# Optimization experiments

Measured on AMD Instinct MI355X. Metric: run time of the kernel, lower is better.

The kernel has to match this reference:

```python
import jax, jax.numpy as jnp
import numpy as np

B, N, DN = 8, 4096, 64
E = 1048576
H, DM = 128, 64   # message MLP: 2*DN -> H -> DM
HU, F = 128, 64   # node-update MLP: DN+DM -> HU -> F


def setup_inputs() -> dict:
    key = jax.random.key(0)
    ks = jax.random.split(key, 13)
    inp = {
        'node_feats': jax.random.normal(ks[0], (B, N, DN), dtype=jnp.float32),
        'edge_b': jax.random.randint(ks[1], (E,), 0, B, dtype=jnp.int32),
        'edge_src': jax.random.randint(ks[2], (E,), 0, N, dtype=jnp.int32),
        'edge_dst': jax.random.randint(ks[3], (E,), 0, N, dtype=jnp.int32),
        'edge_vals': jax.random.uniform(ks[4], (E,), dtype=jnp.float32),
        # message MLP params (Dense-relu, Dense-linear)
        'Wm1': jax.random.normal(ks[5], (2 * DN, H), dtype=jnp.float32) / np.sqrt(2 * DN),
        'bm1': jnp.zeros((H,), jnp.float32),
        'Wm2': jax.random.normal(ks[6], (H, DM), dtype=jnp.float32) / np.sqrt(H),
        'bm2': jnp.zeros((DM,), jnp.float32),
        # node-update MLP params
        'Wu1': jax.random.normal(ks[7], (DN + DM, HU), dtype=jnp.float32) / np.sqrt(DN + DM),
        'bu1': jnp.zeros((HU,), jnp.float32),
        'Wu2': jax.random.normal(ks[8], (HU, F), dtype=jnp.float32) / np.sqrt(HU),
        'bu2': jnp.zeros((F,), jnp.float32),
    }
    return inp


def reference(node_feats, edge_b, edge_src, edge_dst, edge_vals,
              Wm1, bm1, Wm2, bm2, Wu1, bu1, Wu2, bu2):
    # --- create messages: gather src/target feats per edge ---
    src_feats = node_feats[edge_b, edge_src]            # (E, DN)
    tgt_feats = node_feats[edge_b, edge_dst]            # (E, DN)
    feats = jnp.concatenate([src_feats, tgt_feats], axis=-1)  # (E, 2*DN)
    h = jax.nn.relu(feats @ Wm1 + bm1)
    messages = h @ Wm2 + bm2                            # (E, DM)

    # --- gather (scatter) messages: weighted ragged segment-mean ---
    weighted = messages * edge_vals[:, None]            # (E, DM)
    seg = edge_b * N + edge_src                          # rowids b*max_N + src
    sums = jax.ops.segment_sum(weighted, seg, num_segments=B * N)
    counts = jax.ops.segment_sum(jnp.ones((E,), weighted.dtype), seg,
                                 num_segments=B * N)
    gathered = sums / jnp.maximum(counts, 1.0)[:, None]  # mean; 0 for empty rows
    gathered = gathered.reshape(B, N, DM)

    # --- update nodes ---
    upd_in = jnp.concatenate([node_feats, gathered], axis=-1)  # (B, N, DN+DM)
    hu = jax.nn.relu(upd_in @ Wu1 + bu1)
    updated = hu @ Wu2 + bu2                            # (B, N, F)
    return updated
```

## Files before the change

kernel.cpp:

```cpp
#include <hip/hip_runtime.h>

#define NB 8
#define NN 4096
#define DNF 64
#define NEDGE 1048576
#define DM 64
#define FF 64

#define NBKT2 2048
#define SPB2 16
#define NXCD 8
#define SUBCAP 176
#define OVFCAP 32768

using f32x4 = __attribute__((ext_vector_type(4))) float;
using s16x8 = __attribute__((ext_vector_type(8))) short;

__device__ __forceinline__ unsigned short f2b(float f) {
    union { float f; unsigned u; } v; v.f = f;
    unsigned r = (v.u + 0x7fffu + ((v.u >> 16) & 1u)) >> 16;
    return (unsigned short)r;
}
__device__ __forceinline__ float uif(unsigned u) {
    union { unsigned u; float f; } v; v.u = u;
    return v.f;
}

__device__ __forceinline__ void pack_one(const float* __restrict__ W,
                                         unsigned short* __restrict__ out,
                                         int K, int Ncols, int idx) {
    int j = idx & 7;
    int lane = (idx >> 3) & 63;
    int frag = idx >> 9;
    int KS = K >> 5;
    int ks = frag % KS;
    int nt = frag / KS;
    int k = ks * 32 + ((lane >> 4) << 3) + j;
    int col = nt * 16 + (lane & 15);
    out[idx] = f2b(W[k * Ncols + col]);
}

__global__ void pack_all(const float* __restrict__ Wm1, const float* __restrict__ Wm2,
                         const float* __restrict__ Wu1, const float* __restrict__ Wu2,
                         unsigned short* __restrict__ Qw, unsigned short* __restrict__ Pw,
                         unsigned short* __restrict__ Wm2p,
                         unsigned short* __restrict__ Wu1p, unsigned short* __restrict__ Wu2p) {
    int idx = blockIdx.x * 256 + threadIdx.x;
    if (idx < 8192)        pack_one(Wm1,              Qw,   64, 128, idx);
    else if (idx < 16384)  pack_one(Wm1 + 64 * 128,   Pw,   64, 128, idx - 8192);
    else if (idx < 24576)  pack_one(Wm2,              Wm2p, 128, 64, idx - 16384);
    else if (idx < 40960)  pack_one(Wu1,              Wu1p, 128, 128, idx - 24576);
    else                   pack_one(Wu2,              Wu2p, 128, 64, idx - 40960);
}

__global__ void pack_weights(const float* __restrict__ W, unsigned short* __restrict__ out,
                             int K, int Ncols) {
    int idx = blockIdx.x * 256 + threadIdx.x;
    if (idx >= K * Ncols) return;
    pack_one(W, out, K, Ncols, idx);
}

__launch_bounds__(256, 4)
__global__ void precompute_pq(const float* __restrict__ X,
                              const unsigned short* __restrict__ Qw,
                              const unsigned short* __restrict__ Pw,
                              const float* __restrict__ b1,
                              unsigned short* __restrict__ Qp,
                              unsigned short* __restrict__ Pp) {
    __shared__ unsigned short A[64][72];
    const int tid = threadIdx.x;
    const int g0 = blockIdx.x * 64;
    for (int i = 0; i < 16; ++i) {
        int idx = i * 256 + tid;
        int node = idx >> 6;
        int f = idx & 63;
        A[node][f] = f2b(X[(size_t)(g0 + node) * DNF + f]);
    }
    __syncthreads();
    const int wave = tid >> 6, lane = tid & 63;
    const int lr = lane & 15, lq = lane >> 4;
    const int arow = wave * 16 + lr;
    s16x8 a[2];
#pragma unroll
    for (int ks = 0; ks < 2; ++ks)
        a[ks] = *reinterpret_cast<const s16x8*>(&A[arow][ks * 32 + lq * 8]);
#pragma unroll
    for (int nt = 0; nt < 8; ++nt) {
        f32x4 accQ = {0.f, 0.f, 0.f, 0.f};
        f32x4 accP = {0.f, 0.f, 0.f, 0.f};
#pragma unroll
        for (int ks = 0; ks < 2; ++ks) {
            s16x8 bq = *reinterpret_cast<const s16x8*>(&Qw[(((nt << 1) + ks) * 64 + lane) * 8]);
            s16x8 bp = *reinterpret_cast<const s16x8*>(&Pw[(((nt << 1) + ks) * 64 + lane) * 8]);
            accQ = __builtin_amdgcn_mfma_f32_16x16x32_bf16(a[ks], bq, accQ, 0, 0, 0);
            accP = __builtin_amdgcn_mfma_f32_16x16x32_bf16(a[ks], bp, accP, 0, 0, 0);
        }
        int col = nt * 16 + lr;
        float bias = b1[col];
#pragma unroll
        for (int j = 0; j < 4; ++j) {
            int row = g0 + wave * 16 + lq * 4 + j;
            Qp[(size_t)row * 128 + col] = f2b(accQ[j] + bias);
            Pp[(size_t)row * 128 + col] = f2b(accP[j]);
        }
    }
}

__launch_bounds__(256, 8)
__global__ void scatter_xcd(const int* __restrict__ eb, const int* __restrict__ esrc,
                            const int* __restrict__ edst, const float* __restrict__ evals,
                            unsigned* __restrict__ gcurP, unsigned* __restrict__ payslot,
                            unsigned* __restrict__ ovf_cnt, unsigned* __restrict__ ovf_seg,
                            unsigned* __restrict__ ovf_pay) {
    unsigned xcd;
    asm volatile("s_getreg_b32 %0, hwreg(HW_REG_XCC_ID)" : "=s"(xcd));
    xcd &= (NXCD - 1);
    const int t0 = blockIdx.x * 1024 + threadIdx.x;
    int seg[4]; unsigned pk[4];
#pragma unroll
    for (int k = 0; k < 4; ++k) {
        int e = t0 + k * 256;
        seg[k] = eb[e] * NN + esrc[e];
        unsigned wq = (unsigned)fminf(evals[e] * 8192.0f + 0.5f, 8191.0f);
        pk[k] = (unsigned)edst[e] | (wq << 12) | ((unsigned)(seg[k] & 15) << 25);
    }
    unsigned pos[4];
#pragma unroll
    for (int k = 0; k < 4; ++k)
        pos[k] = atomicAdd(&gcurP[(xcd * NBKT2 + (seg[k] >> 4)) * 16], 1u);
#pragma unroll
    for (int k = 0; k < 4; ++k) {
        if (pos[k] < (unsigned)SUBCAP) {
            payslot[((size_t)(seg[k] >> 4) * NXCD + xcd) * SUBCAP + pos[k]] = pk[k];
        } else {
            unsigned o = atomicAdd(ovf_cnt, 1u);
            if (o < (unsigned)OVFCAP) { ovf_seg[o] = (unsigned)seg[k]; ovf_pay[o] = pk[k]; }
        }
    }
}

__launch_bounds__(256, 6)
__global__ void bucket16_fused(const unsigned short* __restrict__ Qp,
                               const unsigned short* __restrict__ Pp,
                               const unsigned* __restrict__ payslot,
                               const unsigned* __restrict__ gcurP,
                               const unsigned* __restrict__ ovf_cnt,
                               const unsigned* __restrict__ ovf_seg,
                               const unsigned* __restrict__ ovf_pay,
                               const unsigned short* __restrict__ Wm2p,
                               const float* __restrict__ b2m,
                               const float* __restrict__ X,
                               const unsigned short* __restrict__ Wu1p,
                               const float* __restrict__ bu1,
                               const unsigned short* __restrict__ Wu2p,
                               const float* __restrict__ bu2,
                               float* __restrict__ out) {
    __shared__ unsigned raw[NXCD * SUBCAP];
    __shared__ unsigned sorted[NXCD * SUBCAP];
    __shared__ unsigned short S[16][136];
    __shared__ unsigned short A1[16][136];
    __shared__ unsigned short Hs[16][136];
    __shared__ unsigned h4[4][16];
    __shared__ unsigned curb4[4][16];
    __shared__ unsigned offs[17];
    __shared__ unsigned cx[NXCD];
    __shared__ float SW[16], SC[16];
    const int tid = threadIdx.x, wv = tid >> 6, lane = tid & 63;
    const int bkt = (blockIdx.x & 7) * 256 + (blockIdx.x >> 3);
    const int node0 = bkt * SPB2;
    const int rowbase = (bkt >> 8) << 12;
    const unsigned novf = ovf_cnt[0];

#pragma unroll
    for (int i = 0; i < 4; ++i) {
        int idx = i * 256 + tid;
        int row = idx >> 6, f = idx & 63;
        A1[row][f] = f2b(X[(size_t)(node0 + row) * DNF + f]);
    }
    if (tid < 64) ((unsigned*)h4)[tid] = 0;
    if (tid < NXCD) cx[tid] = min(gcurP[(tid * NBKT2 + bkt) * 16], (unsigned)SUBCAP);
    __syncthreads();
#pragma unroll
    for (int xi = 0; xi < 2; ++xi) {
        int x = wv * 2 + xi;
        unsigned c = cx[x];
        for (unsigned i = lane; i < c; i += 64) {
            unsigned v = payslot[((size_t)bkt * NXCD + x) * SUBCAP + i];
            raw[x * SUBCAP + i] = v;
            atomicAdd(&h4[wv][(v >> 25) & 15u], 1u);
        }
    }
    __syncthreads();
    if (tid < 16) {
        int xx = (int)(h4[0][tid] + h4[1][tid] + h4[2][tid] + h4[3][tid]);
#pragma unroll
        for (int o = 1; o < 16; o <<= 1) {
            int y = __shfl_up(xx, o);
            if (tid >= o) xx += y;
        }
        offs[tid + 1] = (unsigned)xx;
        if (tid == 0) offs[0] = 0;
    }
    __syncthreads();
    if (tid < 64) {
        int w = tid >> 4, b = tid & 15;
        unsigned base = offs[b];
        for (int w2 = 0; w2 < w; ++w2) base += h4[w2][b];
        curb4[w][b] = base;
    }
    __syncthreads();
#pragma unroll
    for (int xi = 0; xi < 2; ++xi) {
        int x = wv * 2 + xi;
        unsigned c = cx[x];
        for (unsigned i = lane; i < c; i += 64) {
            unsigned v = raw[x * SUBCAP + i];
            unsigned pos = atomicAdd(&curb4[wv][(v >> 25) & 15u], 1u);
            sorted[pos] = v;
        }
    }
    __syncthreads();

    const unsigned* P32 = reinterpret_cast<const unsigned*>(Pp);
    const unsigned* Q32 = reinterpret_cast<const unsigned*>(Qp);
    const unsigned* Pb = P32 + (size_t)rowbase * 64 + lane;
    for (int si = 0; si < 4; ++si) {
        const int lo = wv * 4 + si;
        const int seg = node0 + lo;
        const unsigned s0 = offs[lo], s1 = offs[lo + 1];
        unsigned qv = Q32[(size_t)seg * 64 + lane];
        float q0 = uif(qv << 16);
        float q1 = uif(qv & 0xffff0000u);
        float acc0 = 0.f, acc1 = 0.f;
        unsigned scnt = s1 - s0;

        float wl = 0.f;
        for (unsigned i = s0 + lane; i < s1; i += 64)
            wl += (float)((sorted[i] >> 12) & 8191u);
        for (int m2 = 1; m2 < 64; m2 <<= 1) wl += __shfl_xor(wl, m2);
        float wsum = wl * (1.0f / 8192.0f);

        for (unsigned bse = s0; bse < s1; bse += 8) {
            unsigned pv[8]; float wf[8];
#pragma unroll
            for (int k = 0; k < 8; ++k) {
                unsigned idx = bse + (unsigned)k;
                unsigned c = (idx < s1) ? sorted[idx] : 0u;
                wf[k] = (float)((c >> 12) & 8191u) * (1.0f / 8192.0f);
                pv[k] = Pb[(size_t)(c & 0xfffu) * 64];
            }
#pragma unroll
            for (int k = 0; k < 8; ++k) {
                float p0 = uif(pv[k] << 16);
                float p1 = uif(pv[k] & 0xffff0000u);
                acc0 = fmaf(wf[k], fmaxf(q0 + p0, 0.f), acc0);
                acc1 = fmaf(wf[k], fmaxf(q1 + p1, 0.f), acc1);
            }
        }
        if (novf > 0) {
            unsigned ncl = min(novf, (unsigned)OVFCAP);
            for (unsigned i = 0; i < ncl; ++i) {
                if (ovf_seg[i] == (unsigned)seg) {
                    unsigned c = ovf_pay[i];
                    float w = (float)((c >> 12) & 8191u) * (1.0f / 8192.0f);
                    unsigned pv = Pb[(size_t)(c & 0xfffu) * 64];
                    acc0 = fmaf(w, fmaxf(q0 + uif(pv << 16), 0.f), acc0);
                    acc1 = fmaf(w, fmaxf(q1 + uif(pv & 0xffff0000u), 0.f), acc1);
                    wsum += w;
                    scnt += 1;
                }
            }
        }
        unsigned sp = (unsigned)f2b(acc0) | ((unsigned)f2b(acc1) << 16);
        *reinterpret_cast<unsigned*>(&S[lo][2 * lane]) = sp;
        if (lane == 0) {
            SW[lo] = wsum;
            SC[lo] = 1.0f / (float)max(scnt, 1u);
        }
    }
    __syncthreads();

    const int lr = lane & 15, lq = lane >> 4;
    {
        s16x8 a[4];
#pragma unroll
        for (int ks = 0; ks < 4; ++ks)
            a[ks] = *reinterpret_cast<const s16x8*>(&S[lr][ks * 32 + lq * 8]);
        f32x4 acc = {0.f, 0.f, 0.f, 0.f};
#pragma unroll
        for (int ks = 0; ks < 4; ++ks) {
            s16x8 bf = *reinterpret_cast<const s16x8*>(&Wm2p[(((wv << 2) + ks) * 64 + lane) * 8]);
            acc = __builtin_amdgcn_mfma_f32_16x16x32_bf16(a[ks], bf, acc, 0, 0, 0);
        }
        float bb = b2m[wv * 16 + lr];
#pragma unroll
        for (int j = 0; j < 4; ++j) {
            int r = lq * 4 + j;
            float g = (acc[j] + SW[r] * bb) * SC[r];
            A1[r][64 + wv * 16 + lr] = f2b(g);
        }
    }
    __syncthreads();

    {
        s16x8 a1[4];
#pragma unroll
        for (int ks = 0; ks < 4; ++ks)
            a1[ks] = *reinterpret_cast<const s16x8*>(&A1[lr][ks * 32 + lq * 8]);
#pragma unroll
        for (int t = 0; t < 2; ++t) {
            int nt = wv * 2 + t;
            f32x4 acc = {0.f, 0.f, 0.f, 0.f};
#pragma unroll
            for (int ks = 0; ks < 4; ++ks) {
                s16x8 bf = *reinterpret_cast<const s16x8*>(&Wu1p[(((nt << 2) + ks) * 64 + lane) * 8]);
                acc = __builtin_amdgcn_mfma_f32_16x16x32_bf16(a1[ks], bf, acc, 0, 0, 0);
            }
            float bias = bu1[nt * 16 + lr];
#pragma unroll
            for (int j = 0; j < 4; ++j) {
                float hh = fmaxf(acc[j] + bias, 0.f);
                Hs[lq * 4 + j][nt * 16 + lr] = f2b(hh);
            }
        }
    }
    __syncthreads();

    {
        s16x8 a2[4];
#pragma unroll
        for (int ks = 0; ks < 4; ++ks)
            a2[ks] = *reinterpret_cast<const s16x8*>(&Hs[lr][ks * 32 + lq * 8]);
        f32x4 acc = {0.f, 0.f, 0.f, 0.f};
#pragma unroll
        for (int ks = 0; ks < 4; ++ks) {
            s16x8 bf = *reinterpret_cast<const s16x8*>(&Wu2p[(((wv << 2) + ks) * 64 + lane) * 8]);
            acc = __builtin_amdgcn_mfma_f32_16x16x32_bf16(a2[ks], bf, acc, 0, 0, 0);
        }
        float bias = bu2[wv * 16 + lr];
#pragma unroll
        for (int j = 0; j < 4; ++j)
            out[(size_t)(node0 + lq * 4 + j) * FF + wv * 16 + lr] = acc[j] + bias;
    }
}


template<int SCALE>
__launch_bounds__(256, 4)
__global__ void node_kernel(const float* __restrict__ node_feats,
                            const float* __restrict__ sums, const float* __restrict__ counts,
                            const unsigned short* __restrict__ W1p, const float* __restrict__ b1,
                            const unsigned short* __restrict__ W2p, const float* __restrict__ b2,
                            float* __restrict__ out) {
    __shared__ unsigned short A1[64][136];
    __shared__ unsigned short Hs[64][136];
    const int tid = threadIdx.x;
    const int g0 = blockIdx.x * 64;
    for (int i = 0; i < 16; ++i) {
        int idx = i * 256 + tid;
        int node = idx >> 6;
        int p = idx & 63;
        int g = g0 + node;
        float2 v;
        if (p < 32) {
            v = *reinterpret_cast<const float2*>(node_feats + (size_t)g * DNF + 2 * p);
        } else {
            float2 s = *reinterpret_cast<const float2*>(sums + (size_t)g * DM + 2 * p - 64);
            if (SCALE) {
                float scale = 1.0f / fmaxf(counts[g], 1.0f);
                s.x *= scale; s.y *= scale;
            }
            v = s;
        }
        unsigned packed = (unsigned)f2b(v.x) | ((unsigned)f2b(v.y) << 16);
        *reinterpret_cast<unsigned*>(&A1[node][2 * p]) = packed;
    }
    __syncthreads();
    const int wave = tid >> 6, lane = tid & 63;
    const int lr = lane & 15, lq = lane >> 4;
    const int arow = wave * 16 + lr;
    s16x8 a[4];
#pragma unroll
    for (int ks = 0; ks < 4; ++ks)
        a[ks] = *reinterpret_cast<const s16x8*>(&A1[arow][ks * 32 + lq * 8]);
#pragma unroll
    for (int nt = 0; nt < 8; ++nt) {
        f32x4 acc = {0.f, 0.f, 0.f, 0.f};
#pragma unroll
        for (int ks = 0; ks < 4; ++ks) {
            s16x8 bf = *reinterpret_cast<const s16x8*>(&W1p[(((nt << 2) + ks) * 64 + lane) * 8]);
            acc = __builtin_amdgcn_mfma_f32_16x16x32_bf16(a[ks], bf, acc, 0, 0, 0);
        }
        float bias = b1[nt * 16 + lr];
#pragma unroll
        for (int j = 0; j < 4; ++j) {
            float h = acc[j] + bias;
            h = h > 0.f ? h : 0.f;
            Hs[wave * 16 + lq * 4 + j][nt * 16 + lr] = f2b(h);
        }
    }
    s16x8 a2[4];
#pragma unroll
    for (int ks = 0; ks < 4; ++ks)
        a2[ks] = *reinterpret_cast<const s16x8*>(&Hs[arow][ks * 32 + lq * 8]);
#pragma unroll
    for (int nt = 0; nt < 4; ++nt) {
        f32x4 acc = {0.f, 0.f, 0.f, 0.f};
#pragma unroll
        for (int ks = 0; ks < 4; ++ks) {
            s16x8 bf = *reinterpret_cast<const s16x8*>(&W2p[(((nt << 2) + ks) * 64 + lane) * 8]);
            acc = __builtin_amdgcn_mfma_f32_16x16x32_bf16(a2[ks], bf, acc, 0, 0, 0);
        }
        float bias = b2[nt * 16 + lr];
#pragma unroll
        for (int j = 0; j < 4; ++j) {
            int g = g0 + wave * 16 + lq * 4 + j;
            out[(size_t)g * FF + nt * 16 + lr] = acc[j] + bias;
        }
    }
}

__launch_bounds__(256, 4)
__global__ void edge_kernel(const float* __restrict__ node_feats,
                            const int* __restrict__ eb, const int* __restrict__ esrc,
                            const int* __restrict__ edst, const float* __restrict__ evals,
                            const unsigned short* __restrict__ W1p, const float* __restrict__ b1,
                            const unsigned short* __restrict__ W2p, const float* __restrict__ b2,
                            float* __restrict__ sums, float* __restrict__ counts) {
    __shared__ unsigned short A1[64][136];
    __shared__ unsigned short Hs[64][136];
    const int tid = threadIdx.x;
    const int e0 = blockIdx.x * 64;
    if (tid < 64) {
        int e = e0 + tid;
        atomicAdd(&counts[eb[e] * NN + esrc[e]], 1.0f);
    }
    for (int i = 0; i < 16; ++i) {
        int idx = i * 256 + tid;
        int edge = idx >> 6;
        int p = idx & 63;
        int e = e0 + edge;
        int b = eb[e];
        const float* row;
        if (p < 32) row = node_feats + ((size_t)b * NN + esrc[e]) * DNF;
        else        row = node_feats + ((size_t)b * NN + edst[e]) * DNF - 64;
        float2 v = *reinterpret_cast<const float2*>(row + 2 * p);
        unsigned packed = (unsigned)f2b(v.x) | ((unsigned)f2b(v.y) << 16);
        *reinterpret_cast<unsigned*>(&A1[edge][2 * p]) = packed;
    }
    __syncthreads();
    const int wave = tid >> 6, lane = tid & 63;
    const int lr = lane & 15, lq = lane >> 4;
    const int arow = wave * 16 + lr;
    s16x8 a[4];
#pragma unroll
    for (int ks = 0; ks < 4; ++ks)
        a[ks] = *reinterpret_cast<const s16x8*>(&A1[arow][ks * 32 + lq * 8]);
#pragma unroll
    for (int nt = 0; nt < 8; ++nt) {
        f32x4 acc = {0.f, 0.f, 0.f, 0.f};
#pragma unroll
        for (int ks = 0; ks < 4; ++ks) {
            s16x8 bf = *reinterpret_cast<const s16x8*>(&W1p[(((nt << 2) + ks) * 64 + lane) * 8]);
            acc = __builtin_amdgcn_mfma_f32_16x16x32_bf16(a[ks], bf, acc, 0, 0, 0);
        }
        float bias = b1[nt * 16 + lr];
#pragma unroll
        for (int j = 0; j < 4; ++j) {
            float h = acc[j] + bias;
            h = h > 0.f ? h : 0.f;
            Hs[wave * 16 + lq * 4 + j][nt * 16 + lr] = f2b(h);
        }
    }
    s16x8 a2[4];
#pragma unroll
    for (int ks = 0; ks < 4; ++ks)
        a2[ks] = *reinterpret_cast<const s16x8*>(&Hs[arow][ks * 32 + lq * 8]);
    float ev[4]; int seg4[4];
#pragma unroll
    for (int j = 0; j < 4; ++j) {
        int r = e0 + wave * 16 + lq * 4 + j;
        ev[j] = evals[r];
        seg4[j] = eb[r] * NN + esrc[r];
    }
#pragma unroll
    for (int nt = 0; nt < 4; ++nt) {
        f32x4 acc = {0.f, 0.f, 0.f, 0.f};
#pragma unroll
        for (int ks = 0; ks < 4; ++ks) {
            s16x8 bf = *reinterpret_cast<const s16x8*>(&W2p[(((nt << 2) + ks) * 64 + lane) * 8]);
            acc = __builtin_amdgcn_mfma_f32_16x16x32_bf16(a2[ks], bf, acc, 0, 0, 0);
        }
        float bias = b2[nt * 16 + lr];
#pragma unroll
        for (int j = 0; j < 4; ++j) {
            float m = (acc[j] + bias) * ev[j];
            atomicAdd(&sums[(size_t)seg4[j] * DM + nt * 16 + lr], m);
        }
    }
}

extern "C" void kernel_launch(void* const* d_in, const int* in_sizes, int n_in,
                              void* d_out, int out_size, void* d_ws, size_t ws_size,
                              hipStream_t stream) {
    const float* node_feats = (const float*)d_in[0];
    const int*   eb    = (const int*)d_in[1];
    const int*   esrc  = (const int*)d_in[2];
    const int*   edst  = (const int*)d_in[3];
    const float* evals = (const float*)d_in[4];
    const float* Wm1 = (const float*)d_in[5];
    const float* bm1 = (const float*)d_in[6];
    const float* Wm2 = (const float*)d_in[7];
    const float* bm2 = (const float*)d_in[8];
    const float* Wu1 = (const float*)d_in[9];
    const float* bu1 = (const float*)d_in[10];
    const float* Wu2 = (const float*)d_in[11];
    const float* bu2 = (const float*)d_in[12];
    float* out = (float*)d_out;
    char* ws = (char*)d_ws;

    const size_t NEED = 29720704;
    if (ws_size >= NEED) {
        unsigned short* Qp      = (unsigned short*)(ws);
        unsigned short* Pp      = (unsigned short*)(ws + 8388608);
        unsigned*       payslot = (unsigned*)(ws + 16777216);
        unsigned*       gcurP   = (unsigned*)(ws + 28311552);
        unsigned*       ovf_cnt = (unsigned*)(ws + 29360128);
        unsigned*       ovf_seg = (unsigned*)(ws + 29360256);
        unsigned*       ovf_pay = (unsigned*)(ws + 29491328);
        unsigned short* Qw      = (unsigned short*)(ws + 29622400);
        unsigned short* Pw      = (unsigned short*)(ws + 29638784);
        unsigned short* Wu1p    = (unsigned short*)(ws + 29655168);
        unsigned short* Wu2p    = (unsigned short*)(ws + 29687936);
        unsigned short* Wm2p    = (unsigned short*)(ws + 29704320);

        hipMemsetAsync(gcurP, 0, 1048576 + 128, stream);
        pack_all<<<192, 256, 0, stream>>>(Wm1, Wm2, Wu1, Wu2, Qw, Pw, Wm2p, Wu1p, Wu2p);
        precompute_pq<<<512, 256, 0, stream>>>(node_feats, Qw, Pw, bm1, Qp, Pp);
        scatter_xcd<<<NEDGE / 1024, 256, 0, stream>>>(eb, esrc, edst, evals,
                                                      gcurP, payslot, ovf_cnt, ovf_seg, ovf_pay);
        bucket16_fused<<<NBKT2, 256, 0, stream>>>(Qp, Pp, payslot, gcurP,
                                                  ovf_cnt, ovf_seg, ovf_pay,
                                                  Wm2p, bm2, node_feats,
                                                  Wu1p, bu1, Wu2p, bu2, out);
    } else {
        float* counts          = (float*)ws;
        unsigned short* W1p    = (unsigned short*)(ws + 131072);
        unsigned short* W2p    = (unsigned short*)(ws + 163840);
        unsigned short* Wu1p   = (unsigned short*)(ws + 180224);
        unsigned short* Wu2p   = (unsigned short*)(ws + 212992);
        hipMemsetAsync(d_out, 0, (size_t)out_size * sizeof(float), stream);
        hipMemsetAsync(counts, 0, 32768 * sizeof(float), stream);
        pack_weights<<<64, 256, 0, stream>>>(Wm1, W1p, 128, 128);
        pack_weights<<<32, 256, 0, stream>>>(Wm2, W2p, 128, 64);
        pack_weights<<<64, 256, 0, stream>>>(Wu1, Wu1p, 128, 128);
        pack_weights<<<32, 256, 0, stream>>>(Wu2, Wu2p, 128, 64);
        edge_kernel<<<NEDGE / 64, 256, 0, stream>>>(node_feats, eb, esrc, edst, evals,
                                                    W1p, bm1, W2p, bm2, out, counts);
        node_kernel<1><<<(NB * NN) / 64, 256, 0, stream>>>(node_feats, out, counts,
                                                           Wu1p, bu1, Wu2p, bu2, out);
    }
}
```

Baseline: 118.9 us.

## Fuse edge scatter with P/Q precompute into one launch; scalarize edge gather loop

New measurement: 111.3 us. 6.4% less time.

```diff
diff --git a/kernel.cpp b/kernel.cpp
--- a/kernel.cpp
+++ b/kernel.cpp
@@ -12,8 +12,10 @@
 #define NXCD 8
 #define SUBCAP 176
 #define OVFCAP 32768
+#define SCATBLK 2048
 
 using f32x4 = __attribute__((ext_vector_type(4))) float;
+using f32x2 = __attribute__((ext_vector_type(2))) float;
 using s16x8 = __attribute__((ext_vector_type(8))) short;
 
 __device__ __forceinline__ unsigned short f2b(float f) {
@@ -60,81 +62,81 @@
     pack_one(W, out, K, Ncols, idx);
 }
 
-__launch_bounds__(256, 4)
-__global__ void precompute_pq(const float* __restrict__ X,
-                              const unsigned short* __restrict__ Qw,
-                              const unsigned short* __restrict__ Pw,
-                              const float* __restrict__ b1,
-                              unsigned short* __restrict__ Qp,
-                              unsigned short* __restrict__ Pp) {
+__launch_bounds__(256, 6)
+__global__ void scatter_pq(const int* __restrict__ eb, const int* __restrict__ esrc,
+                           const int* __restrict__ edst, const float* __restrict__ evals,
+                           unsigned* __restrict__ gcurP, unsigned* __restrict__ payslot,
+                           unsigned* __restrict__ ovf_cnt, unsigned* __restrict__ ovf_seg,
+                           unsigned* __restrict__ ovf_pay,
+                           const float* __restrict__ X,
+                           const unsigned short* __restrict__ Qw,
+                           const unsigned short* __restrict__ Pw,
+                           const float* __restrict__ b1,
+                           unsigned short* __restrict__ Qp,
+                           unsigned short* __restrict__ Pp) {
     __shared__ unsigned short A[64][72];
-    const int tid = threadIdx.x;
-    const int g0 = blockIdx.x * 64;
-    for (int i = 0; i < 16; ++i) {
-        int idx = i * 256 + tid;
-        int node = idx >> 6;
-        int f = idx & 63;
-        A[node][f] = f2b(X[(size_t)(g0 + node) * DNF + f]);
-    }
-    __syncthreads();
-    const int wave = tid >> 6, lane = tid & 63;
-    const int lr = lane & 15, lq = lane >> 4;
-    const int arow = wave * 16 + lr;
-    s16x8 a[2];
-#pragma unroll
-    for (int ks = 0; ks < 2; ++ks)
-        a[ks] = *reinterpret_cast<const s16x8*>(&A[arow][ks * 32 + lq * 8]);
-#pragma unroll
-    for (int nt = 0; nt < 8; ++nt) {
-        f32x4 accQ = {0.f, 0.f, 0.f, 0.f};
-        f32x4 accP = {0.f, 0.f, 0.f, 0.f};
-#pragma unroll
-        for (int ks = 0; ks < 2; ++ks) {
-            s16x8 bq = *reinterpret_cast<const s16x8*>(&Qw[(((nt << 1) + ks) * 64 + lane) * 8]);
-            s16x8 bp = *reinterpret_cast<const s16x8*>(&Pw[(((nt << 1) + ks) * 64 + lane) * 8]);
-            accQ = __builtin_amdgcn_mfma_f32_16x16x32_bf16(a[ks], bq, accQ, 0, 0, 0);
-            accP = __builtin_amdgcn_mfma_f32_16x16x32_bf16(a[ks], bp, accP, 0, 0, 0);
-        }
-        int col = nt * 16 + lr;
-        float bias = b1[col];
-#pragma unroll
-        for (int j = 0; j < 4; ++j) {
-            int row = g0 + wave * 16 + lq * 4 + j;
-            Qp[(size_t)row * 128 + col] = f2b(accQ[j] + bias);
-            Pp[(size_t)row * 128 + col] = f2b(accP[j]);
-        }
-    }
-}
-
-__launch_bounds__(256, 8)
-__global__ void scatter_xcd(const int* __restrict__ eb, const int* __restrict__ esrc,
-                            const int* __restrict__ edst, const float* __restrict__ evals,
-                            unsigned* __restrict__ gcurP, unsigned* __restrict__ payslot,
-                            unsigned* __restrict__ ovf_cnt, unsigned* __restrict__ ovf_seg,
-                            unsigned* __restrict__ ovf_pay) {
-    unsigned xcd;
-    asm volatile("s_getreg_b32 %0, hwreg(HW_REG_XCC_ID)" : "=s"(xcd));
-    xcd &= (NXCD - 1);
-    const int t0 = blockIdx.x * 1024 + threadIdx.x;
-    int seg[4]; unsigned pk[4];
-#pragma unroll
-    for (int k = 0; k < 4; ++k) {
-        int e = t0 + k * 256;
-        seg[k] = eb[e] * NN + esrc[e];
-        unsigned wq = (unsigned)fminf(evals[e] * 8192.0f + 0.5f, 8191.0f);
-        pk[k] = (unsigned)edst[e] | (wq << 12) | ((unsigned)(seg[k] & 15) << 25);
-    }
-    unsigned pos[4];
-#pragma unroll
-    for (int k = 0; k < 4; ++k)
-        pos[k] = atomicAdd(&gcurP[(xcd * NBKT2 + (seg[k] >> 4)) * 16], 1u);
-#pragma unroll
-    for (int k = 0; k < 4; ++k) {
-        if (pos[k] < (unsigned)SUBCAP) {
-            payslot[((size_t)(seg[k] >> 4) * NXCD + xcd) * SUBCAP + pos[k]] = pk[k];
-        } else {
-            unsigned o = atomicAdd(ovf_cnt, 1u);
-            if (o < (unsigned)OVFCAP) { ovf_seg[o] = (unsigned)seg[k]; ovf_pay[o] = pk[k]; }
+    if (blockIdx.x < SCATBLK) {
+        unsigned xcd;
+        asm volatile("s_getreg_b32 %0, hwreg(HW_REG_XCC_ID)" : "=s"(xcd));
+        xcd &= (NXCD - 1);
+        const int t0 = blockIdx.x * 512 + threadIdx.x;
+        int seg[2]; unsigned pk[2];
+#pragma unroll
+        for (int k = 0; k < 2; ++k) {
+            int e = t0 + k * 256;
+            seg[k] = eb[e] * NN + esrc[e];
+            unsigned wq = (unsigned)fminf(evals[e] * 8192.0f + 0.5f, 8191.0f);
+            pk[k] = (unsigned)edst[e] | (wq << 12) | ((unsigned)(seg[k] & 15) << 25);
+        }
+        unsigned pos[2];
+#pragma unroll
+        for (int k = 0; k < 2; ++k)
+            pos[k] = atomicAdd(&gcurP[((int)xcd * NBKT2 + (seg[k] >> 4)) * 16], 1u);
+#pragma unroll
+        for (int k = 0; k < 2; ++k) {
+            if (pos[k] < (unsigned)SUBCAP) {
+                payslot[((size_t)(seg[k] >> 4) * NXCD + xcd) * SUBCAP + pos[k]] = pk[k];
+            } else {
+                unsigned o = atomicAdd(ovf_cnt, 1u);
+                if (o < (unsigned)OVFCAP) { ovf_seg[o] = (unsigned)seg[k]; ovf_pay[o] = pk[k]; }
+            }
+        }
+    } else {
+        const int tid = threadIdx.x;
+        const int g0 = (blockIdx.x - SCATBLK) * 64;
+        for (int i = 0; i < 16; ++i) {
+            int idx = i * 256 + tid;
+            int node = idx >> 6;
+            int f = idx & 63;
+            A[node][f] = f2b(X[(size_t)(g0 + node) * DNF + f]);
+        }
+        __syncthreads();
+        const int wave = tid >> 6, lane = tid & 63;
+        const int lr = lane & 15, lq = lane >> 4;
+        const int arow = wave * 16 + lr;
+        s16x8 a[2];
+#pragma unroll
+        for (int ks = 0; ks < 2; ++ks)
+            a[ks] = *reinterpret_cast<const s16x8*>(&A[arow][ks * 32 + lq * 8]);
+#pragma unroll
+        for (int nt = 0; nt < 8; ++nt) {
+            f32x4 accQ = {0.f, 0.f, 0.f, 0.f};
+            f32x4 accP = {0.f, 0.f, 0.f, 0.f};
+#pragma unroll
+            for (int ks = 0; ks < 2; ++ks) {
+                s16x8 bq = *reinterpret_cast<const s16x8*>(&Qw[(((nt << 1) + ks) * 64 + lane) * 8]);
+                s16x8 bp = *reinterpret_cast<const s16x8*>(&Pw[(((nt << 1) + ks) * 64 + lane) * 8]);
+                accQ = __builtin_amdgcn_mfma_f32_16x16x32_bf16(a[ks], bq, accQ, 0, 0, 0);
+                accP = __builtin_amdgcn_mfma_f32_16x16x32_bf16(a[ks], bp, accP, 0, 0, 0);
+            }
+            int col = nt * 16 + lr;
+            float bias = b1[col];
+#pragma unroll
+            for (int j = 0; j < 4; ++j) {
+                int row = g0 + wave * 16 + lq * 4 + j;
+                Qp[(size_t)row * 128 + col] = f2b(accQ[j] + bias);
+                Pp[(size_t)row * 128 + col] = f2b(accP[j]);
+            }
         }
     }
 }
@@ -223,38 +225,39 @@
 
     const unsigned* P32 = reinterpret_cast<const unsigned*>(Pp);
     const unsigned* Q32 = reinterpret_cast<const unsigned*>(Qp);
-    const unsigned* Pb = P32 + (size_t)rowbase * 64 + lane;
+    const unsigned* PbS = P32 + (size_t)rowbase * 64;
     for (int si = 0; si < 4; ++si) {
         const int lo = wv * 4 + si;
         const int seg = node0 + lo;
         const unsigned s0 = offs[lo], s1 = offs[lo + 1];
         unsigned qv = Q32[(size_t)seg * 64 + lane];
-        float q0 = uif(qv << 16);
-        float q1 = uif(qv & 0xffff0000u);
-        float acc0 = 0.f, acc1 = 0.f;
+        f32x2 q2 = { uif(qv << 16), uif(qv & 0xffff0000u) };
+        f32x2 acc2 = { 0.f, 0.f };
         unsigned scnt = s1 - s0;
 
         float wl = 0.f;
         for (unsigned i = s0 + lane; i < s1; i += 64)
             wl += (float)((sorted[i] >> 12) & 8191u);
         for (int m2 = 1; m2 < 64; m2 <<= 1) wl += __shfl_xor(wl, m2);
-        float wsum = wl * (1.0f / 8192.0f);
+        float wsum = wl;
 
         for (unsigned bse = s0; bse < s1; bse += 8) {
             unsigned pv[8]; float wf[8];
 #pragma unroll
             for (int k = 0; k < 8; ++k) {
                 unsigned idx = bse + (unsigned)k;
-                unsigned c = (idx < s1) ? sorted[idx] : 0u;
-                wf[k] = (float)((c >> 12) & 8191u) * (1.0f / 8192.0f);
-                pv[k] = Pb[(size_t)(c & 0xfffu) * 64];
+                unsigned cu = (idx < s1) ? sorted[idx] : 0u;
+                int ci = __builtin_amdgcn_readfirstlane((int)cu);
+                wf[k] = (float)(unsigned)((ci >> 12) & 8191);
+                int row = ci & 0xfff;
+                pv[k] = PbS[(size_t)row * 64 + lane];
             }
 #pragma unroll
             for (int k = 0; k < 8; ++k) {
-                float p0 = uif(pv[k] << 16);
-                float p1 = uif(pv[k] & 0xffff0000u);
-                acc0 = fmaf(wf[k], fmaxf(q0 + p0, 0.f), acc0);
-                acc1 = fmaf(wf[k], fmaxf(q1 + p1, 0.f), acc1);
+                f32x2 p2 = { uif(pv[k] << 16), uif(pv[k] & 0xffff0000u) };
+                f32x2 h2 = q2 + p2;
+                h2 = __builtin_elementwise_max(h2, (f32x2){0.f, 0.f});
+                acc2 += wf[k] * h2;
             }
         }
         if (novf > 0) {
@@ -262,20 +265,22 @@
             for (unsigned i = 0; i < ncl; ++i) {
                 if (ovf_seg[i] == (unsigned)seg) {
                     unsigned c = ovf_pay[i];
-                    float w = (float)((c >> 12) & 8191u) * (1.0f / 8192.0f);
-                    unsigned pv = Pb[(size_t)(c & 0xfffu) * 64];
-                    acc0 = fmaf(w, fmaxf(q0 + uif(pv << 16), 0.f), acc0);
-                    acc1 = fmaf(w, fmaxf(q1 + uif(pv & 0xffff0000u), 0.f), acc1);
+                    float w = (float)((c >> 12) & 8191u);
+                    unsigned pv = PbS[(size_t)(c & 0xfffu) * 64 + lane];
+                    f32x2 p2 = { uif(pv << 16), uif(pv & 0xffff0000u) };
+                    f32x2 h2 = q2 + p2;
+                    h2 = __builtin_elementwise_max(h2, (f32x2){0.f, 0.f});
+                    acc2 += w * h2;
                     wsum += w;
                     scnt += 1;
                 }
             }
         }
-        unsigned sp = (unsigned)f2b(acc0) | ((unsigned)f2b(acc1) << 16);
+        unsigned sp = (unsigned)f2b(acc2.x) | ((unsigned)f2b(acc2.y) << 16);
         *reinterpret_cast<unsigned*>(&S[lo][2 * lane]) = sp;
         if (lane == 0) {
             SW[lo] = wsum;
-            SC[lo] = 1.0f / (float)max(scnt, 1u);
+            SC[lo] = (1.0f / 8192.0f) / (float)max(scnt, 1u);
         }
     }
     __syncthreads();
@@ -536,9 +541,9 @@
 
         hipMemsetAsync(gcurP, 0, 1048576 + 128, stream);
         pack_all<<<192, 256, 0, stream>>>(Wm1, Wm2, Wu1, Wu2, Qw, Pw, Wm2p, Wu1p, Wu2p);
-        precompute_pq<<<512, 256, 0, stream>>>(node_feats, Qw, Pw, bm1, Qp, Pp);
-        scatter_xcd<<<NEDGE / 1024, 256, 0, stream>>>(eb, esrc, edst, evals,
-                                                      gcurP, payslot, ovf_cnt, ovf_seg, ovf_pay);
+        scatter_pq<<<SCATBLK + 512, 256, 0, stream>>>(eb, esrc, edst, evals,
+                                                      gcurP, payslot, ovf_cnt, ovf_seg, ovf_pay,
+                                                      node_feats, Qw, Pw, bm1, Qp, Pp);
         bucket16_fused<<<NBKT2, 256, 0, stream>>>(Qp, Pp, payslot, gcurP,
                                                   ovf_cnt, ovf_seg, ovf_pay,
                                                   Wm2p, bm2, node_feats,
```
